# Optimization experiments

Measured on AMD Instinct MI355X. Metric: run time of the kernel, lower is better.

## Reference

```python
import jax, jax.numpy as jnp
import numpy as np

DIM = 768
H = 12        # query heads
HKV = 4       # kv heads
G = H // HKV  # GQA group size
HD = 64       # head dim
CAP = 50.0    # soft cap (Gemma-2 style)
EPS = 1e-6
SCALE = HD ** -0.5
B, T, S = 1, 128, 256


def setup_inputs() -> dict:
    key = jax.random.key(0)
    ks = jax.random.split(key, 5)
    s = DIM ** -0.5
    x = jax.random.normal(ks[0], (B, T, S, DIM), jnp.float32)
    Wq = jax.random.normal(ks[1], (DIM, H * HD), jnp.float32) * s
    Wk = jax.random.normal(ks[2], (DIM, HKV * HD), jnp.float32) * s
    Wv = jax.random.normal(ks[3], (DIM, HKV * HD), jnp.float32) * s
    Wo = jax.random.normal(ks[4], (H * HD, DIM), jnp.float32) * s
    q_norm_w = jnp.ones((HD,), jnp.float32)
    k_norm_w = jnp.ones((HD,), jnp.float32)
    return {"x": x, "Wq": Wq, "Wk": Wk, "Wv": Wv, "Wo": Wo,
            "q_norm_w": q_norm_w, "k_norm_w": k_norm_w}


def _rmsnorm(x, w):
    # x: (..., HD)
    return x * jax.lax.rsqrt(jnp.mean(x * x, axis=-1, keepdims=True) + EPS) * w


def reference(x, Wq, Wk, Wv, Wo, q_norm_w, k_norm_w):
    b, t, s, d = x.shape
    n = b * s
    # fold spatial into batch: temporal attention per spatial position
    xf = x.transpose(0, 2, 1, 3).reshape(n, t, d)             # (N, T, D)
    q = (xf @ Wq).reshape(n, t, H, HD).transpose(0, 2, 1, 3)   # (N, H, T, hd)
    k = (xf @ Wk).reshape(n, t, HKV, HD).transpose(0, 2, 1, 3) # (N, Hkv, T, hd)
    v = (xf @ Wv).reshape(n, t, HKV, HD).transpose(0, 2, 1, 3)
    # QKNorm (per-head RMSNorm on head_dim)
    q = _rmsnorm(q, q_norm_w)
    k = _rmsnorm(k, k_norm_w)
    # GQA without materializing repeated K/V: split q heads into (Hkv, G)
    # (repeat_interleave maps query head h -> kv head h // G, matching kv*G+g)
    qg = q.reshape(n, HKV, G, t, HD)
    attn = jnp.einsum('bkgtd,bksd->bkgts', qg, k) * SCALE      # (N, Hkv, G, T, T)
    attn = CAP * jnp.tanh(attn / CAP)                          # soft cap
    causal = jnp.triu(jnp.ones((t, t), bool), 1)               # True above diag
    attn = jnp.where(causal, -jnp.inf, attn)
    attn = jax.nn.softmax(attn, axis=-1)
    out = jnp.einsum('bkgts,bksd->bkgtd', attn, v)             # (N, Hkv, G, T, hd)
    out = out.reshape(n, H, t, HD).transpose(0, 2, 1, 3).reshape(n, t, H * HD)
    out = out @ Wo                                             # (N, T, D)
    return out.reshape(b, s, t, d).transpose(0, 2, 1, 3)        # (B, T, S, D)
```

## Files before the change

kernel.cpp:

```cpp
#include <hip/hip_runtime.h>
#include <stdint.h>
#include <stddef.h>

#define DIM 768
#define NH  12
#define NKV 4
#define HD  64
#define TT  128
#define NS  256

typedef __attribute__((ext_vector_type(8))) short bf16x8;
typedef __attribute__((ext_vector_type(4))) float f32x4;
typedef __attribute__((ext_vector_type(4))) unsigned int u32x4;
typedef __attribute__((ext_vector_type(2))) unsigned int u32x2;

__device__ __forceinline__ unsigned short f2bf(float f) {
  union { float f; unsigned int u; } v; v.f = f;
  return (unsigned short)((v.u + 0x7FFFu + ((v.u >> 16) & 1u)) >> 16);
}

__device__ __forceinline__ void gload_lds16(const void* g, void* l) {
  __builtin_amdgcn_global_load_lds(
      (const __attribute__((address_space(1))) unsigned int*)g,
      (__attribute__((address_space(3))) unsigned int*)l, 16, 0, 0);
}

__global__ __launch_bounds__(256)
void prep_kernel(const float* __restrict__ x, const float* __restrict__ Wq,
                 const float* __restrict__ Wk, const float* __restrict__ Wv,
                 const float* __restrict__ Wo, unsigned short* __restrict__ Wt,
                 unsigned short* __restrict__ WoT, unsigned short* __restrict__ xb) {
  const int b = blockIdx.x, tid = threadIdx.x;
  if (b < 6144) {
    int idx = b * 256 + tid;
    const int n1 = 1280 * DIM;
    if (idx < n1) {
      int c = idx / DIM, kk = idx - c * DIM;
      float v;
      if (c < 768)       v = Wq[kk * 768 + c];
      else if (c < 1024) v = Wk[kk * 256 + (c - 768)];
      else               v = Wv[kk * 256 + (c - 1024)];
      Wt[idx] = f2bf(v);
    } else {
      int i2 = idx - n1;
      int c = i2 / DIM, kk = i2 - c * DIM;
      WoT[i2] = f2bf(Wo[kk * 768 + c]);
    }
  } else {
    int g = (b - 6144) * 256 + tid;
    int r = g / 192;
    int k = g - r * 192;
    int t = r >> 8, n = r & 255;
    f32x4 f = *reinterpret_cast<const f32x4*>(x + (size_t)g * 4);
    u32x2 pk;
    pk[0] = (unsigned)f2bf(f[0]) | ((unsigned)f2bf(f[1]) << 16);
    pk[1] = (unsigned)f2bf(f[2]) | ((unsigned)f2bf(f[3]) << 16);
    *reinterpret_cast<u32x2*>(xb + (size_t)((n << 7) + t) * DIM + k * 4) = pk;
  }
}

__global__ __launch_bounds__(512, 2)
void qkv_kernel(const unsigned short* __restrict__ xb, const float* __restrict__ qnw,
                const float* __restrict__ knw, const unsigned short* __restrict__ Wt,
                unsigned short* __restrict__ qb, unsigned short* __restrict__ kb,
                unsigned short* __restrict__ vTb) {
  extern __shared__ unsigned short lds[];
  const int b = blockIdx.x;
  const int x8 = b & 7, idx = b >> 3;
  const int cbt = idx % 5;
  const int n   = (idx / 5) * 8 + x8;
  const int tid = threadIdx.x;
  const int wave = tid >> 6, lane = tid & 63;
  const int cl = lane & 15, rowg = lane >> 4;
  const int wmw = wave >> 2, wn = wave & 3;
  const int l8 = lane >> 3, s8 = lane & 7;
  const int col0 = cbt * 256;
  const unsigned short* asrc = xb + (size_t)(n * TT + l8) * DIM + (s8 ^ l8) * 8;
  const unsigned short* bsrc = Wt + (size_t)(col0 + l8) * DIM + (s8 ^ l8) * 8;
  const int swzr = (cl & 7) << 4;
  f32x4 acc[4][4] = {};

#define QKV_STAGE(buf, ko)                                                  \
  {                                                                         \
    unsigned short* Ad = lds + (buf) * 24576;                               \
    unsigned short* Bd = Ad + 8192;                                         \
    _Pragma("unroll")                                                       \
    for (int i = 0; i < 2; ++i) {                                           \
      const int r0 = i * 64 + wave * 8;                                     \
      gload_lds16(asrc + (size_t)r0 * DIM + (ko), Ad + r0 * 64);            \
    }                                                                       \
    _Pragma("unroll")                                                       \
    for (int i = 0; i < 4; ++i) {                                           \
      const int r0 = i * 64 + wave * 8;                                     \
      gload_lds16(bsrc + (size_t)r0 * DIM + (ko), Bd + r0 * 64);            \
    }                                                                       \
  }

  QKV_STAGE(0, 0);
  __syncthreads();
  for (int kt = 0; kt < 12; ++kt) {
    if (kt < 11) QKV_STAGE((kt + 1) & 1, (kt + 1) * 64);
    const char* Ab = (const char*)(lds + (kt & 1) * 24576);
    const char* Bb = Ab + 16384;
    #pragma unroll
    for (int ks = 0; ks < 2; ++ks) {
      bf16x8 a[4], bb[4];
      #pragma unroll
      for (int m = 0; m < 4; ++m)
        a[m] = *(const bf16x8*)(Ab + (wmw * 64 + m * 16 + cl) * 128 + ((ks * 64 + rowg * 16) ^ swzr));
      #pragma unroll
      for (int nn = 0; nn < 4; ++nn)
        bb[nn] = *(const bf16x8*)(Bb + (wn * 64 + nn * 16 + cl) * 128 + ((ks * 64 + rowg * 16) ^ swzr));
      #pragma unroll
      for (int m = 0; m < 4; ++m)
        #pragma unroll
        for (int nn = 0; nn < 4; ++nn)
          acc[m][nn] = __builtin_amdgcn_mfma_f32_16x16x32_bf16(a[m], bb[nn], acc[m][nn], 0, 0, 0);
    }
    __syncthreads();
  }

  if (cbt == 4) {
    const int kv = wn;
    unsigned short* dst = vTb + (size_t)((n * NKV + kv) * HD) * TT;
    #pragma unroll
    for (int m = 0; m < 4; ++m) {
      const int tb = wmw * 64 + m * 16 + rowg * 4;
      #pragma unroll
      for (int nn = 0; nn < 4; ++nn) {
        const int d = nn * 16 + cl;
        u32x2 pk;
        pk[0] = (unsigned)f2bf(acc[m][nn][0]) | ((unsigned)f2bf(acc[m][nn][1]) << 16);
        pk[1] = (unsigned)f2bf(acc[m][nn][2]) | ((unsigned)f2bf(acc[m][nn][3]) << 16);
        *reinterpret_cast<u32x2*>(dst + (size_t)d * TT + tb) = pk;
      }
    }
  } else {
    const int isq = (cbt < 3);
    const float* nw = isq ? qnw : knw;
    float wfrag[4];
    #pragma unroll
    for (int nn = 0; nn < 4; ++nn) wfrag[nn] = nw[nn * 16 + cl];
    const float rs = isq ? 0.125f : 1.0f;
    unsigned short* dst;
    if (isq) { const int hh = cbt * 4 + wn; dst = qb + (size_t)(n * NH + hh) * TT * HD; }
    else     { const int kv = wn;           dst = kb + (size_t)(n * NKV + kv) * TT * HD; }
    #pragma unroll
    for (int m = 0; m < 4; ++m) {
      #pragma unroll
      for (int j = 0; j < 4; ++j) {
        const int t = wmw * 64 + m * 16 + rowg * 4 + j;
        float ss = 0.f;
        #pragma unroll
        for (int nn = 0; nn < 4; ++nn) { float v = acc[m][nn][j]; ss += v * v; }
        #pragma unroll
        for (int dlt = 1; dlt < 16; dlt <<= 1) ss += __shfl_xor(ss, dlt);
        const float r = rsqrtf(ss * (1.f / 64.f) + 1e-6f) * rs;
        #pragma unroll
        for (int nn = 0; nn < 4; ++nn)
          dst[(size_t)t * HD + nn * 16 + cl] = f2bf(acc[m][nn][j] * r * wfrag[nn]);
      }
    }
  }
#undef QKV_STAGE
}

__global__ __launch_bounds__(256)
void attn_kernel(const unsigned short* __restrict__ qb, const unsigned short* __restrict__ kb,
                 const unsigned short* __restrict__ vTb, unsigned short* __restrict__ ab) {
  extern __shared__ char smem[];
  unsigned short (*Ks)[72]   = reinterpret_cast<unsigned short (*)[72]>(smem);
  unsigned short (*Vts)[136] = reinterpret_cast<unsigned short (*)[136]>(smem + 18432);
  unsigned short (*Pl)[136]  = reinterpret_cast<unsigned short (*)[136]>(smem + 35840);
  const int b = blockIdx.x;
  const int x8 = b & 7, idx = b >> 3;
  const int kv = idx & 3;
  const int n  = (idx >> 2) * 8 + x8;
  const int tid = threadIdx.x, wave = tid >> 6, lane = tid & 63;
  const int cl = lane & 15, rowg = lane >> 4;

  const unsigned short* ksrc = kb + (size_t)(n * NKV + kv) * TT * HD;
  const unsigned short* vsrc = vTb + (size_t)(n * NKV + kv) * HD * TT;
  #pragma unroll
  for (int i = 0; i < 4; ++i) {
    int c = tid + 256 * i, r = c >> 3, seg = c & 7;
    *reinterpret_cast<u32x4*>(&Ks[r][seg * 8]) = *reinterpret_cast<const u32x4*>(ksrc + c * 8);
  }
  #pragma unroll
  for (int i = 0; i < 4; ++i) {
    int c = tid + 256 * i, r = c >> 4, seg = c & 15;
    *reinterpret_cast<u32x4*>(&Vts[r][seg * 8]) = *reinterpret_cast<const u32x4*>(vsrc + c * 8);
  }
  __syncthreads();

  for (int hh = 0; hh < 3; ++hh) {
    const int h = kv * 3 + hh;
    const unsigned short* qsrc = qb + (size_t)(n * NH + h) * TT * HD;
    f32x4 sc[2][8] = {};
    #pragma unroll
    for (int ks = 0; ks < 2; ++ks) {
      bf16x8 a[2], bbf[8];
      #pragma unroll
      for (int m = 0; m < 2; ++m)
        a[m] = *reinterpret_cast<const bf16x8*>(
            qsrc + (size_t)(wave * 32 + m * 16 + cl) * HD + ks * 32 + rowg * 8);
      #pragma unroll
      for (int nn = 0; nn < 8; ++nn)
        bbf[nn] = *reinterpret_cast<const bf16x8*>(&Ks[nn * 16 + cl][ks * 32 + rowg * 8]);
      #pragma unroll
      for (int m = 0; m < 2; ++m)
        #pragma unroll
        for (int nn = 0; nn < 8; ++nn)
          sc[m][nn] = __builtin_amdgcn_mfma_f32_16x16x32_bf16(a[m], bbf[nn], sc[m][nn], 0, 0, 0);
    }
    #pragma unroll
    for (int m = 0; m < 2; ++m) {
      #pragma unroll
      for (int j = 0; j < 4; ++j) {
        const int rowv = wave * 32 + m * 16 + rowg * 4 + j;
        float mx = -__builtin_inff();
        #pragma unroll
        for (int nn = 0; nn < 8; ++nn) {
          float s = sc[m][nn][j];
          float e = __expf(s * 0.04f);
          s = 50.f - 100.f * __builtin_amdgcn_rcpf(e + 1.f);
          if (nn * 16 + cl > rowv) s = -__builtin_inff();
          sc[m][nn][j] = s;
          mx = fmaxf(mx, s);
        }
        #pragma unroll
        for (int d = 1; d < 16; d <<= 1) mx = fmaxf(mx, __shfl_xor(mx, d));
        float sum = 0.f;
        #pragma unroll
        for (int nn = 0; nn < 8; ++nn) {
          float e = __expf(sc[m][nn][j] - mx);
          sc[m][nn][j] = e;
          sum += e;
        }
        #pragma unroll
        for (int d = 1; d < 16; d <<= 1) sum += __shfl_xor(sum, d);
        const float inv = __builtin_amdgcn_rcpf(sum);
        #pragma unroll
        for (int nn = 0; nn < 8; ++nn)
          Pl[rowv][nn * 16 + cl] = f2bf(sc[m][nn][j] * inv);
      }
    }
    __syncthreads();
    f32x4 o[2][4] = {};
    #pragma unroll
    for (int ks = 0; ks < 4; ++ks) {
      bf16x8 a[2], bbf[4];
      #pragma unroll
      for (int m = 0; m < 2; ++m)
        a[m] = *reinterpret_cast<const bf16x8*>(&Pl[wave * 32 + m * 16 + cl][ks * 32 + rowg * 8]);
      #pragma unroll
      for (int nn = 0; nn < 4; ++nn)
        bbf[nn] = *reinterpret_cast<const bf16x8*>(&Vts[nn * 16 + cl][ks * 32 + rowg * 8]);
      #pragma unroll
      for (int m = 0; m < 2; ++m)
        #pragma unroll
        for (int nn = 0; nn < 4; ++nn)
          o[m][nn] = __builtin_amdgcn_mfma_f32_16x16x32_bf16(a[m], bbf[nn], o[m][nn], 0, 0, 0);
    }
    unsigned short* dst = ab + (size_t)n * TT * DIM + h * HD;
    #pragma unroll
    for (int m = 0; m < 2; ++m)
      #pragma unroll
      for (int j = 0; j < 4; ++j) {
        int t = wave * 32 + m * 16 + rowg * 4 + j;
        #pragma unroll
        for (int nn = 0; nn < 4; ++nn)
          dst[(size_t)t * DIM + nn * 16 + cl] = f2bf(o[m][nn][j]);
      }
    __syncthreads();
  }
}

__global__ __launch_bounds__(512, 2)
void out_kernel(const unsigned short* __restrict__ ab, const unsigned short* __restrict__ WoT,
                float* __restrict__ out) {
  extern __shared__ unsigned short lds[];
  const int b = blockIdx.x;
  const int x8 = b & 7, idx = b >> 3;
  const int cbt = idx % 3;
  const int n   = (idx / 3) * 8 + x8;
  const int tid = threadIdx.x;
  const int wave = tid >> 6, lane = tid & 63;
  const int cl = lane & 15, rowg = lane >> 4;
  const int wmw = wave >> 2, wn = wave & 3;
  const int l8 = lane >> 3, s8 = lane & 7;
  const unsigned short* asrc = ab  + (size_t)(n * TT + l8) * DIM + (s8 ^ l8) * 8;
  const unsigned short* bsrc = WoT + (size_t)(cbt * 256 + l8) * DIM + (s8 ^ l8) * 8;
  const int swzr = (cl & 7) << 4;
  f32x4 acc[4][4] = {};

#define OUT_STAGE(buf, ko)                                                  \
  {                                                                         \
    unsigned short* Ad = lds + (buf) * 24576;                               \
    unsigned short* Bd = Ad + 8192;                                         \
    _Pragma("unroll")                                                       \
    for (int i = 0; i < 2; ++i) {                                           \
      const int r0 = i * 64 + wave * 8;                                     \
      gload_lds16(asrc + (size_t)r0 * DIM + (ko), Ad + r0 * 64);            \
    }                                                                       \
    _Pragma("unroll")                                                       \
    for (int i = 0; i < 4; ++i) {                                           \
      const int r0 = i * 64 + wave * 8;                                     \
      gload_lds16(bsrc + (size_t)r0 * DIM + (ko), Bd + r0 * 64);            \
    }                                                                       \
  }

  OUT_STAGE(0, 0);
  __syncthreads();
  for (int kt = 0; kt < 12; ++kt) {
    if (kt < 11) OUT_STAGE((kt + 1) & 1, (kt + 1) * 64);
    const char* Ab = (const char*)(lds + (kt & 1) * 24576);
    const char* Bb = Ab + 16384;
    #pragma unroll
    for (int ks = 0; ks < 2; ++ks) {
      bf16x8 a[4], bb[4];
      #pragma unroll
      for (int m = 0; m < 4; ++m)
        a[m] = *(const bf16x8*)(Ab + (wmw * 64 + m * 16 + cl) * 128 + ((ks * 64 + rowg * 16) ^ swzr));
      #pragma unroll
      for (int nn = 0; nn < 4; ++nn)
        bb[nn] = *(const bf16x8*)(Bb + (wn * 64 + nn * 16 + cl) * 128 + ((ks * 64 + rowg * 16) ^ swzr));
      #pragma unroll
      for (int m = 0; m < 4; ++m)
        #pragma unroll
        for (int nn = 0; nn < 4; ++nn)
          acc[m][nn] = __builtin_amdgcn_mfma_f32_16x16x32_bf16(a[m], bb[nn], acc[m][nn], 0, 0, 0);
    }
    __syncthreads();
  }
  #pragma unroll
  for (int m = 0; m < 4; ++m)
    #pragma unroll
    for (int j = 0; j < 4; ++j) {
      int t = wmw * 64 + m * 16 + rowg * 4 + j;
      #pragma unroll
      for (int nn = 0; nn < 4; ++nn)
        out[(size_t)(t * NS + n) * DIM + cbt * 256 + wn * 64 + nn * 16 + cl] = acc[m][nn][j];
    }
#undef OUT_STAGE
}

extern "C" void kernel_launch(void* const* d_in, const int* in_sizes, int n_in,
                              void* d_out, int out_size, void* d_ws, size_t ws_size,
                              hipStream_t stream) {
  const float* x   = (const float*)d_in[0];
  const float* Wq  = (const float*)d_in[1];
  const float* Wk  = (const float*)d_in[2];
  const float* Wv  = (const float*)d_in[3];
  const float* Wo  = (const float*)d_in[4];
  const float* qnw = (const float*)d_in[5];
  const float* knw = (const float*)d_in[6];
  (void)in_sizes; (void)n_in; (void)out_size;

  char* ws = (char*)d_ws;
  unsigned short* Wt  = (unsigned short*)(ws + 0);
  unsigned short* WoT = (unsigned short*)(ws + 1966080);
  unsigned short* qb  = (unsigned short*)(ws + 3145728);
  unsigned short* kb  = (unsigned short*)(ws + 53477376);
  unsigned short* vTb = (unsigned short*)(ws + 70254592);
  unsigned short* ab  = (unsigned short*)(ws + 87031808);
  unsigned short* xb  = ab;
  if (ws_size < 137363456) return;

  hipFuncSetAttribute(reinterpret_cast<const void*>(qkv_kernel),
                      hipFuncAttributeMaxDynamicSharedMemorySize, 98304);
  hipFuncSetAttribute(reinterpret_cast<const void*>(out_kernel),
                      hipFuncAttributeMaxDynamicSharedMemorySize, 98304);
  hipFuncSetAttribute(reinterpret_cast<const void*>(attn_kernel),
                      hipFuncAttributeMaxDynamicSharedMemorySize, 70656);

  prep_kernel<<<30720, 256, 0, stream>>>(x, Wq, Wk, Wv, Wo, Wt, WoT, xb);
  qkv_kernel<<<1280, 512, 98304, stream>>>(xb, qnw, knw, Wt, qb, kb, vTb);
  attn_kernel<<<1024, 256, 70656, stream>>>(qb, kb, vTb, ab);
  out_kernel<<<768, 512, 98304, stream>>>(ab, WoT, (float*)d_out);
}
```

Before: 219.5 us.

## Triple-buffer GEMM K-loop with one barrier; stage Q/K epilogue through LDS

Both projection GEMMs (QKV and output) move from a double-buffered K-loop with two __syncthreads per step to a three-stage LDS ring. Each step waits with an explicit s_waitcnt vmcnt and uses one s_barrier, so global-to-LDS loads run two tiles ahead and one barrier per iteration is removed. The Q/K normalized epilogue now writes its bf16 results into LDS and then copies them out with 16-byte coalesced stores, replacing scattered 2-byte global stores. Dynamic LDS rises from 96KB to 144KB per block, which rules out running two blocks per CU and depends on hand-written vmcnt counts matching the per-stage load count.

```diff
diff --git a/kernel.cpp b/kernel.cpp
--- a/kernel.cpp
+++ b/kernel.cpp
@@ -74,9 +74,8 @@
   const int cl = lane & 15, rowg = lane >> 4;
   const int wmw = wave >> 2, wn = wave & 3;
   const int l8 = lane >> 3, s8 = lane & 7;
-  const int col0 = cbt * 256;
   const unsigned short* asrc = xb + (size_t)(n * TT + l8) * DIM + (s8 ^ l8) * 8;
-  const unsigned short* bsrc = Wt + (size_t)(col0 + l8) * DIM + (s8 ^ l8) * 8;
+  const unsigned short* bsrc = Wt + (size_t)(cbt * 256 + l8) * DIM + (s8 ^ l8) * 8;
   const int swzr = (cl & 7) << 4;
   f32x4 acc[4][4] = {};
 
@@ -97,10 +96,15 @@
   }
 
   QKV_STAGE(0, 0);
-  __syncthreads();
+  QKV_STAGE(1, 64);
+  #pragma unroll
   for (int kt = 0; kt < 12; ++kt) {
-    if (kt < 11) QKV_STAGE((kt + 1) & 1, (kt + 1) * 64);
-    const char* Ab = (const char*)(lds + (kt & 1) * 24576);
+    if (kt < 11) asm volatile("s_waitcnt vmcnt(6)" ::: "memory");
+    else         asm volatile("s_waitcnt vmcnt(0)" ::: "memory");
+    __builtin_amdgcn_s_barrier();
+    __builtin_amdgcn_sched_barrier(0);
+    if (kt + 2 < 12) QKV_STAGE((kt + 2) % 3, (kt + 2) * 64);
+    const char* Ab = (const char*)(lds + (kt % 3) * 24576);
     const char* Bb = Ab + 16384;
     #pragma unroll
     for (int ks = 0; ks < 2; ++ks) {
@@ -117,8 +121,9 @@
         for (int nn = 0; nn < 4; ++nn)
           acc[m][nn] = __builtin_amdgcn_mfma_f32_16x16x32_bf16(a[m], bb[nn], acc[m][nn], 0, 0, 0);
     }
-    __syncthreads();
-  }
+  }
+#undef QKV_STAGE
+  __syncthreads();
 
   if (cbt == 4) {
     const int kv = wn;
@@ -142,9 +147,6 @@
     #pragma unroll
     for (int nn = 0; nn < 4; ++nn) wfrag[nn] = nw[nn * 16 + cl];
     const float rs = isq ? 0.125f : 1.0f;
-    unsigned short* dst;
-    if (isq) { const int hh = cbt * 4 + wn; dst = qb + (size_t)(n * NH + hh) * TT * HD; }
-    else     { const int kv = wn;           dst = kb + (size_t)(n * NKV + kv) * TT * HD; }
     #pragma unroll
     for (int m = 0; m < 4; ++m) {
       #pragma unroll
@@ -158,11 +160,18 @@
         const float r = rsqrtf(ss * (1.f / 64.f) + 1e-6f) * rs;
         #pragma unroll
         for (int nn = 0; nn < 4; ++nn)
-          dst[(size_t)t * HD + nn * 16 + cl] = f2bf(acc[m][nn][j] * r * wfrag[nn]);
+          lds[wn * 8192 + t * 64 + nn * 16 + cl] = f2bf(acc[m][nn][j] * r * wfrag[nn]);
       }
     }
-  }
-#undef QKV_STAGE
+    __syncthreads();
+    unsigned short* gdst = isq ? qb + ((size_t)n * NH + cbt * 4) * TT * HD
+                               : kb + (size_t)n * NKV * TT * HD;
+    #pragma unroll
+    for (int i = 0; i < 8; ++i) {
+      const int c = tid + 512 * i;
+      *reinterpret_cast<u32x4*>(gdst + c * 8) = *reinterpret_cast<const u32x4*>(lds + c * 8);
+    }
+  }
 }
 
 __global__ __launch_bounds__(256)
@@ -311,10 +320,15 @@
   }
 
   OUT_STAGE(0, 0);
-  __syncthreads();
+  OUT_STAGE(1, 64);
+  #pragma unroll
   for (int kt = 0; kt < 12; ++kt) {
-    if (kt < 11) OUT_STAGE((kt + 1) & 1, (kt + 1) * 64);
-    const char* Ab = (const char*)(lds + (kt & 1) * 24576);
+    if (kt < 11) asm volatile("s_waitcnt vmcnt(6)" ::: "memory");
+    else         asm volatile("s_waitcnt vmcnt(0)" ::: "memory");
+    __builtin_amdgcn_s_barrier();
+    __builtin_amdgcn_sched_barrier(0);
+    if (kt + 2 < 12) OUT_STAGE((kt + 2) % 3, (kt + 2) * 64);
+    const char* Ab = (const char*)(lds + (kt % 3) * 24576);
     const char* Bb = Ab + 16384;
     #pragma unroll
     for (int ks = 0; ks < 2; ++ks) {
@@ -331,8 +345,8 @@
         for (int nn = 0; nn < 4; ++nn)
           acc[m][nn] = __builtin_amdgcn_mfma_f32_16x16x32_bf16(a[m], bb[nn], acc[m][nn], 0, 0, 0);
     }
-    __syncthreads();
-  }
+  }
+#undef OUT_STAGE
   #pragma unroll
   for (int m = 0; m < 4; ++m)
     #pragma unroll
@@ -342,7 +356,6 @@
       for (int nn = 0; nn < 4; ++nn)
         out[(size_t)(t * NS + n) * DIM + cbt * 256 + wn * 64 + nn * 16 + cl] = acc[m][nn][j];
     }
-#undef OUT_STAGE
 }
 
 extern "C" void kernel_launch(void* const* d_in, const int* in_sizes, int n_in,
@@ -368,14 +381,14 @@
   if (ws_size < 137363456) return;
 
   hipFuncSetAttribute(reinterpret_cast<const void*>(qkv_kernel),
-                      hipFuncAttributeMaxDynamicSharedMemorySize, 98304);
+                      hipFuncAttributeMaxDynamicSharedMemorySize, 147456);
   hipFuncSetAttribute(reinterpret_cast<const void*>(out_kernel),
-                      hipFuncAttributeMaxDynamicSharedMemorySize, 98304);
+                      hipFuncAttributeMaxDynamicSharedMemorySize, 147456);
   hipFuncSetAttribute(reinterpret_cast<const void*>(attn_kernel),
                       hipFuncAttributeMaxDynamicSharedMemorySize, 70656);
 
   prep_kernel<<<30720, 256, 0, stream>>>(x, Wq, Wk, Wv, Wo, Wt, WoT, xb);
-  qkv_kernel<<<1280, 512, 98304, stream>>>(xb, qnw, knw, Wt, qb, kb, vTb);
+  qkv_kernel<<<1280, 512, 147456, stream>>>(xb, qnw, knw, Wt, qb, kb, vTb);
   attn_kernel<<<1024, 256, 70656, stream>>>(qb, kb, vTb, ab);
-  out_kernel<<<768, 512, 98304, stream>>>(ab, WoT, (float*)d_out);
-}
+  out_kernel<<<768, 512, 147456, stream>>>(ab, WoT, (float*)d_out);
+}
```

Result: no change. 223.2 us (+1.7%).

## Fuse x fp32-to-bf16 conversion into QKV GEMM loads and stage Q/K stores via LDS

Applied to the files above, without the earlier changes.

The separate pass in the prep kernel that converted and transposed x to bf16 is removed. The QKV GEMM now reads fp32 x directly with register prefetch, converts it, and writes swizzled bf16 tiles to LDS, while B tiles still use async global-to-LDS loads. This saves a full write and read of the bf16 copy of x. The cost is that each of the five column-tile blocks per position re-reads fp32 x, doubling A-operand bytes per tile. Q/K results are also staged in LDS and written out with coalesced 16-byte stores instead of scattered 2-byte stores.

```diff
diff --git a/kernel.cpp b/kernel.cpp
--- a/kernel.cpp
+++ b/kernel.cpp
@@ -26,41 +26,27 @@
 }
 
 __global__ __launch_bounds__(256)
-void prep_kernel(const float* __restrict__ x, const float* __restrict__ Wq,
-                 const float* __restrict__ Wk, const float* __restrict__ Wv,
-                 const float* __restrict__ Wo, unsigned short* __restrict__ Wt,
-                 unsigned short* __restrict__ WoT, unsigned short* __restrict__ xb) {
-  const int b = blockIdx.x, tid = threadIdx.x;
-  if (b < 6144) {
-    int idx = b * 256 + tid;
-    const int n1 = 1280 * DIM;
-    if (idx < n1) {
-      int c = idx / DIM, kk = idx - c * DIM;
-      float v;
-      if (c < 768)       v = Wq[kk * 768 + c];
-      else if (c < 1024) v = Wk[kk * 256 + (c - 768)];
-      else               v = Wv[kk * 256 + (c - 1024)];
-      Wt[idx] = f2bf(v);
-    } else {
-      int i2 = idx - n1;
-      int c = i2 / DIM, kk = i2 - c * DIM;
-      WoT[i2] = f2bf(Wo[kk * 768 + c]);
-    }
+void prep_kernel(const float* __restrict__ Wq, const float* __restrict__ Wk,
+                 const float* __restrict__ Wv, const float* __restrict__ Wo,
+                 unsigned short* __restrict__ Wt, unsigned short* __restrict__ WoT) {
+  int idx = blockIdx.x * 256 + threadIdx.x;
+  const int n1 = 1280 * DIM;
+  if (idx < n1) {
+    int c = idx / DIM, kk = idx - c * DIM;
+    float v;
+    if (c < 768)       v = Wq[kk * 768 + c];
+    else if (c < 1024) v = Wk[kk * 256 + (c - 768)];
+    else               v = Wv[kk * 256 + (c - 1024)];
+    Wt[idx] = f2bf(v);
   } else {
-    int g = (b - 6144) * 256 + tid;
-    int r = g / 192;
-    int k = g - r * 192;
-    int t = r >> 8, n = r & 255;
-    f32x4 f = *reinterpret_cast<const f32x4*>(x + (size_t)g * 4);
-    u32x2 pk;
-    pk[0] = (unsigned)f2bf(f[0]) | ((unsigned)f2bf(f[1]) << 16);
-    pk[1] = (unsigned)f2bf(f[2]) | ((unsigned)f2bf(f[3]) << 16);
-    *reinterpret_cast<u32x2*>(xb + (size_t)((n << 7) + t) * DIM + k * 4) = pk;
+    int i2 = idx - n1;
+    int c = i2 / DIM, kk = i2 - c * DIM;
+    WoT[i2] = f2bf(Wo[kk * 768 + c]);
   }
 }
 
 __global__ __launch_bounds__(512, 2)
-void qkv_kernel(const unsigned short* __restrict__ xb, const float* __restrict__ qnw,
+void qkv_kernel(const float* __restrict__ x, const float* __restrict__ qnw,
                 const float* __restrict__ knw, const unsigned short* __restrict__ Wt,
                 unsigned short* __restrict__ qb, unsigned short* __restrict__ kb,
                 unsigned short* __restrict__ vTb) {
@@ -74,32 +60,48 @@
   const int cl = lane & 15, rowg = lane >> 4;
   const int wmw = wave >> 2, wn = wave & 3;
   const int l8 = lane >> 3, s8 = lane & 7;
-  const int col0 = cbt * 256;
-  const unsigned short* asrc = xb + (size_t)(n * TT + l8) * DIM + (s8 ^ l8) * 8;
-  const unsigned short* bsrc = Wt + (size_t)(col0 + l8) * DIM + (s8 ^ l8) * 8;
+  const unsigned short* bsrc = Wt + (size_t)(cbt * 256 + l8) * DIM + (s8 ^ l8) * 8;
   const int swzr = (cl & 7) << 4;
+  const int r0 = tid >> 3, s0 = tid & 7;
+  const float* ax0 = x + (size_t)(r0 * NS + n) * DIM + s0 * 8;
+  const float* ax1 = x + (size_t)((r0 + 64) * NS + n) * DIM + s0 * 8;
+  const int wd0 = r0 * 128 + ((s0 * 16) ^ ((r0 & 7) << 4));
+  const int wd1 = (r0 + 64) * 128 + ((s0 * 16) ^ ((r0 & 7) << 4));
   f32x4 acc[4][4] = {};
-
-#define QKV_STAGE(buf, ko)                                                  \
-  {                                                                         \
-    unsigned short* Ad = lds + (buf) * 24576;                               \
-    unsigned short* Bd = Ad + 8192;                                         \
-    _Pragma("unroll")                                                       \
-    for (int i = 0; i < 2; ++i) {                                           \
-      const int r0 = i * 64 + wave * 8;                                     \
-      gload_lds16(asrc + (size_t)r0 * DIM + (ko), Ad + r0 * 64);            \
-    }                                                                       \
-    _Pragma("unroll")                                                       \
-    for (int i = 0; i < 4; ++i) {                                           \
-      const int r0 = i * 64 + wave * 8;                                     \
-      gload_lds16(bsrc + (size_t)r0 * DIM + (ko), Bd + r0 * 64);            \
-    }                                                                       \
-  }
-
-  QKV_STAGE(0, 0);
+  f32x4 aL0, aL1, aL2, aL3;
+
+#define QKV_STAGE_B(bufp, ko) {                                              \
+    unsigned short* Bd = lds + (bufp) * 24576 + 8192;                        \
+    gload_lds16(bsrc + (size_t)(wave * 8) * DIM + (ko), Bd + (wave * 8) * 64);            \
+    gload_lds16(bsrc + (size_t)(64 + wave * 8) * DIM + (ko), Bd + (64 + wave * 8) * 64);  \
+    gload_lds16(bsrc + (size_t)(128 + wave * 8) * DIM + (ko), Bd + (128 + wave * 8) * 64);\
+    gload_lds16(bsrc + (size_t)(192 + wave * 8) * DIM + (ko), Bd + (192 + wave * 8) * 64); }
+#define QKV_A_LOAD(ko) {                                                     \
+    aL0 = *reinterpret_cast<const f32x4*>(ax0 + (ko));                       \
+    aL1 = *reinterpret_cast<const f32x4*>(ax0 + (ko) + 4);                   \
+    aL2 = *reinterpret_cast<const f32x4*>(ax1 + (ko));                       \
+    aL3 = *reinterpret_cast<const f32x4*>(ax1 + (ko) + 4); }
+#define QKV_A_WRITE(bufp) {                                                  \
+    unsigned short* Ad = lds + (bufp) * 24576;                               \
+    u32x4 p0, p1;                                                            \
+    p0[0] = (unsigned)f2bf(aL0[0]) | ((unsigned)f2bf(aL0[1]) << 16);         \
+    p0[1] = (unsigned)f2bf(aL0[2]) | ((unsigned)f2bf(aL0[3]) << 16);         \
+    p0[2] = (unsigned)f2bf(aL1[0]) | ((unsigned)f2bf(aL1[1]) << 16);         \
+    p0[3] = (unsigned)f2bf(aL1[2]) | ((unsigned)f2bf(aL1[3]) << 16);         \
+    p1[0] = (unsigned)f2bf(aL2[0]) | ((unsigned)f2bf(aL2[1]) << 16);         \
+    p1[1] = (unsigned)f2bf(aL2[2]) | ((unsigned)f2bf(aL2[3]) << 16);         \
+    p1[2] = (unsigned)f2bf(aL3[0]) | ((unsigned)f2bf(aL3[1]) << 16);         \
+    p1[3] = (unsigned)f2bf(aL3[2]) | ((unsigned)f2bf(aL3[3]) << 16);         \
+    *reinterpret_cast<u32x4*>((char*)Ad + wd0) = p0;                         \
+    *reinterpret_cast<u32x4*>((char*)Ad + wd1) = p1; }
+
+  QKV_A_LOAD(0);
+  QKV_STAGE_B(0, 0);
+  QKV_A_WRITE(0);
   __syncthreads();
   for (int kt = 0; kt < 12; ++kt) {
-    if (kt < 11) QKV_STAGE((kt + 1) & 1, (kt + 1) * 64);
+    const int nxt = (kt + 1) & 1;
+    if (kt < 11) { QKV_A_LOAD((kt + 1) * 64); QKV_STAGE_B(nxt, (kt + 1) * 64); }
     const char* Ab = (const char*)(lds + (kt & 1) * 24576);
     const char* Bb = Ab + 16384;
     #pragma unroll
@@ -117,8 +119,13 @@
         for (int nn = 0; nn < 4; ++nn)
           acc[m][nn] = __builtin_amdgcn_mfma_f32_16x16x32_bf16(a[m], bb[nn], acc[m][nn], 0, 0, 0);
     }
-    __syncthreads();
-  }
+    if (kt < 11) QKV_A_WRITE(nxt);
+    __syncthreads();
+  }
+#undef QKV_STAGE_B
+#undef QKV_A_LOAD
+#undef QKV_A_WRITE
+  __syncthreads();
 
   if (cbt == 4) {
     const int kv = wn;
@@ -142,9 +149,7 @@
     #pragma unroll
     for (int nn = 0; nn < 4; ++nn) wfrag[nn] = nw[nn * 16 + cl];
     const float rs = isq ? 0.125f : 1.0f;
-    unsigned short* dst;
-    if (isq) { const int hh = cbt * 4 + wn; dst = qb + (size_t)(n * NH + hh) * TT * HD; }
-    else     { const int kv = wn;           dst = kb + (size_t)(n * NKV + kv) * TT * HD; }
+    unsigned short* slab = lds + wn * 8192;
     #pragma unroll
     for (int m = 0; m < 4; ++m) {
       #pragma unroll
@@ -158,11 +163,18 @@
         const float r = rsqrtf(ss * (1.f / 64.f) + 1e-6f) * rs;
         #pragma unroll
         for (int nn = 0; nn < 4; ++nn)
-          dst[(size_t)t * HD + nn * 16 + cl] = f2bf(acc[m][nn][j] * r * wfrag[nn]);
+          slab[t * 64 + nn * 16 + cl] = f2bf(acc[m][nn][j] * r * wfrag[nn]);
       }
     }
-  }
-#undef QKV_STAGE
+    __syncthreads();
+    unsigned short* gdst = isq ? qb + ((size_t)n * NH + cbt * 4) * TT * HD
+                               : kb + (size_t)n * NKV * TT * HD;
+    #pragma unroll
+    for (int i = 0; i < 8; ++i) {
+      const int c = tid + 512 * i;
+      *reinterpret_cast<u32x4*>(gdst + c * 8) = *reinterpret_cast<const u32x4*>(lds + c * 8);
+    }
+  }
 }
 
 __global__ __launch_bounds__(256)
@@ -300,13 +312,13 @@
     unsigned short* Bd = Ad + 8192;                                         \
     _Pragma("unroll")                                                       \
     for (int i = 0; i < 2; ++i) {                                           \
-      const int r0 = i * 64 + wave * 8;                                     \
-      gload_lds16(asrc + (size_t)r0 * DIM + (ko), Ad + r0 * 64);            \
+      const int rr = i * 64 + wave * 8;                                     \
+      gload_lds16(asrc + (size_t)rr * DIM + (ko), Ad + rr * 64);            \
     }                                                                       \
     _Pragma("unroll")                                                       \
     for (int i = 0; i < 4; ++i) {                                           \
-      const int r0 = i * 64 + wave * 8;                                     \
-      gload_lds16(bsrc + (size_t)r0 * DIM + (ko), Bd + r0 * 64);            \
+      const int rr = i * 64 + wave * 8;                                     \
+      gload_lds16(bsrc + (size_t)rr * DIM + (ko), Bd + rr * 64);            \
     }                                                                       \
   }
 
@@ -333,6 +345,7 @@
     }
     __syncthreads();
   }
+#undef OUT_STAGE
   #pragma unroll
   for (int m = 0; m < 4; ++m)
     #pragma unroll
@@ -342,7 +355,6 @@
       for (int nn = 0; nn < 4; ++nn)
         out[(size_t)(t * NS + n) * DIM + cbt * 256 + wn * 64 + nn * 16 + cl] = acc[m][nn][j];
     }
-#undef OUT_STAGE
 }
 
 extern "C" void kernel_launch(void* const* d_in, const int* in_sizes, int n_in,
@@ -364,7 +376,6 @@
   unsigned short* kb  = (unsigned short*)(ws + 53477376);
   unsigned short* vTb = (unsigned short*)(ws + 70254592);
   unsigned short* ab  = (unsigned short*)(ws + 87031808);
-  unsigned short* xb  = ab;
   if (ws_size < 137363456) return;
 
   hipFuncSetAttribute(reinterpret_cast<const void*>(qkv_kernel),
@@ -374,8 +385,8 @@
   hipFuncSetAttribute(reinterpret_cast<const void*>(attn_kernel),
                       hipFuncAttributeMaxDynamicSharedMemorySize, 70656);
 
-  prep_kernel<<<30720, 256, 0, stream>>>(x, Wq, Wk, Wv, Wo, Wt, WoT, xb);
-  qkv_kernel<<<1280, 512, 98304, stream>>>(xb, qnw, knw, Wt, qb, kb, vTb);
+  prep_kernel<<<6144, 256, 0, stream>>>(Wq, Wk, Wv, Wo, Wt, WoT);
+  qkv_kernel<<<1280, 512, 98304, stream>>>(x, qnw, knw, Wt, qb, kb, vTb);
   attn_kernel<<<1024, 256, 70656, stream>>>(qb, kb, vTb, ab);
   out_kernel<<<768, 512, 98304, stream>>>(ab, WoT, (float*)d_out);
 }
```

Measured after the change: 246.1 us. +12.1%, slower.

## Parallelize attention heads across waves instead of a serial per-head loop

Applied to the files above, without the earlier changes.

The attention kernel now runs 6 waves per block, one per (query head of the GQA group, 64-row half), instead of 4 waves looping over the three heads. Each wave gets a private P buffer in LDS, which removes the per-head __syncthreads barriers and the serial head loop. The cost is a much larger LDS footprint (about 140 KB per block), which likely limits the kernel to one block per CU. It also raises per-wave register use, with larger score and output accumulators.

```diff
diff --git a/kernel.cpp b/kernel.cpp
--- a/kernel.cpp
+++ b/kernel.cpp
@@ -74,9 +74,8 @@
   const int cl = lane & 15, rowg = lane >> 4;
   const int wmw = wave >> 2, wn = wave & 3;
   const int l8 = lane >> 3, s8 = lane & 7;
-  const int col0 = cbt * 256;
   const unsigned short* asrc = xb + (size_t)(n * TT + l8) * DIM + (s8 ^ l8) * 8;
-  const unsigned short* bsrc = Wt + (size_t)(col0 + l8) * DIM + (s8 ^ l8) * 8;
+  const unsigned short* bsrc = Wt + (size_t)(cbt * 256 + l8) * DIM + (s8 ^ l8) * 8;
   const int swzr = (cl & 7) << 4;
   f32x4 acc[4][4] = {};
 
@@ -86,13 +85,13 @@
     unsigned short* Bd = Ad + 8192;                                         \
     _Pragma("unroll")                                                       \
     for (int i = 0; i < 2; ++i) {                                           \
-      const int r0 = i * 64 + wave * 8;                                     \
-      gload_lds16(asrc + (size_t)r0 * DIM + (ko), Ad + r0 * 64);            \
+      const int rr = i * 64 + wave * 8;                                     \
+      gload_lds16(asrc + (size_t)rr * DIM + (ko), Ad + rr * 64);            \
     }                                                                       \
     _Pragma("unroll")                                                       \
     for (int i = 0; i < 4; ++i) {                                           \
-      const int r0 = i * 64 + wave * 8;                                     \
-      gload_lds16(bsrc + (size_t)r0 * DIM + (ko), Bd + r0 * 64);            \
+      const int rr = i * 64 + wave * 8;                                     \
+      gload_lds16(bsrc + (size_t)rr * DIM + (ko), Bd + rr * 64);            \
     }                                                                       \
   }
 
@@ -119,6 +118,7 @@
     }
     __syncthreads();
   }
+#undef QKV_STAGE
 
   if (cbt == 4) {
     const int kv = wn;
@@ -162,118 +162,118 @@
       }
     }
   }
-#undef QKV_STAGE
-}
-
-__global__ __launch_bounds__(256)
+}
+
+__global__ __launch_bounds__(384)
 void attn_kernel(const unsigned short* __restrict__ qb, const unsigned short* __restrict__ kb,
                  const unsigned short* __restrict__ vTb, unsigned short* __restrict__ ab) {
   extern __shared__ char smem[];
   unsigned short (*Ks)[72]   = reinterpret_cast<unsigned short (*)[72]>(smem);
   unsigned short (*Vts)[136] = reinterpret_cast<unsigned short (*)[136]>(smem + 18432);
-  unsigned short (*Pl)[136]  = reinterpret_cast<unsigned short (*)[136]>(smem + 35840);
   const int b = blockIdx.x;
   const int x8 = b & 7, idx = b >> 3;
   const int kv = idx & 3;
   const int n  = (idx >> 2) * 8 + x8;
   const int tid = threadIdx.x, wave = tid >> 6, lane = tid & 63;
   const int cl = lane & 15, rowg = lane >> 4;
+  const int h     = kv * 3 + (wave >> 1);
+  const int rbase = (wave & 1) * 64;
 
   const unsigned short* ksrc = kb + (size_t)(n * NKV + kv) * TT * HD;
   const unsigned short* vsrc = vTb + (size_t)(n * NKV + kv) * HD * TT;
-  #pragma unroll
-  for (int i = 0; i < 4; ++i) {
-    int c = tid + 256 * i, r = c >> 3, seg = c & 7;
-    *reinterpret_cast<u32x4*>(&Ks[r][seg * 8]) = *reinterpret_cast<const u32x4*>(ksrc + c * 8);
-  }
-  #pragma unroll
-  for (int i = 0; i < 4; ++i) {
-    int c = tid + 256 * i, r = c >> 4, seg = c & 15;
-    *reinterpret_cast<u32x4*>(&Vts[r][seg * 8]) = *reinterpret_cast<const u32x4*>(vsrc + c * 8);
+  if (tid < 256) {
+    #pragma unroll
+    for (int i = 0; i < 4; ++i) {
+      int c = tid + 256 * i, r = c >> 3, seg = c & 7;
+      *reinterpret_cast<u32x4*>(&Ks[r][seg * 8]) = *reinterpret_cast<const u32x4*>(ksrc + c * 8);
+    }
+    #pragma unroll
+    for (int i = 0; i < 4; ++i) {
+      int c = tid + 256 * i, r = c >> 4, seg = c & 15;
+      *reinterpret_cast<u32x4*>(&Vts[r][seg * 8]) = *reinterpret_cast<const u32x4*>(vsrc + c * 8);
+    }
   }
   __syncthreads();
 
-  for (int hh = 0; hh < 3; ++hh) {
-    const int h = kv * 3 + hh;
-    const unsigned short* qsrc = qb + (size_t)(n * NH + h) * TT * HD;
-    f32x4 sc[2][8] = {};
-    #pragma unroll
-    for (int ks = 0; ks < 2; ++ks) {
-      bf16x8 a[2], bbf[8];
-      #pragma unroll
-      for (int m = 0; m < 2; ++m)
-        a[m] = *reinterpret_cast<const bf16x8*>(
-            qsrc + (size_t)(wave * 32 + m * 16 + cl) * HD + ks * 32 + rowg * 8);
+  const unsigned short* qsrc = qb + (size_t)(n * NH + h) * TT * HD;
+  f32x4 sc[4][8] = {};
+  #pragma unroll
+  for (int ks = 0; ks < 2; ++ks) {
+    bf16x8 a[4], bbf[8];
+    #pragma unroll
+    for (int m = 0; m < 4; ++m)
+      a[m] = *reinterpret_cast<const bf16x8*>(
+          qsrc + (size_t)(rbase + m * 16 + cl) * HD + ks * 32 + rowg * 8);
+    #pragma unroll
+    for (int nn = 0; nn < 8; ++nn)
+      bbf[nn] = *reinterpret_cast<const bf16x8*>(&Ks[nn * 16 + cl][ks * 32 + rowg * 8]);
+    #pragma unroll
+    for (int m = 0; m < 4; ++m)
       #pragma unroll
       for (int nn = 0; nn < 8; ++nn)
-        bbf[nn] = *reinterpret_cast<const bf16x8*>(&Ks[nn * 16 + cl][ks * 32 + rowg * 8]);
-      #pragma unroll
-      for (int m = 0; m < 2; ++m)
-        #pragma unroll
-        for (int nn = 0; nn < 8; ++nn)
-          sc[m][nn] = __builtin_amdgcn_mfma_f32_16x16x32_bf16(a[m], bbf[nn], sc[m][nn], 0, 0, 0);
-    }
-    #pragma unroll
-    for (int m = 0; m < 2; ++m) {
-      #pragma unroll
-      for (int j = 0; j < 4; ++j) {
-        const int rowv = wave * 32 + m * 16 + rowg * 4 + j;
-        float mx = -__builtin_inff();
-        #pragma unroll
-        for (int nn = 0; nn < 8; ++nn) {
-          float s = sc[m][nn][j];
-          float e = __expf(s * 0.04f);
-          s = 50.f - 100.f * __builtin_amdgcn_rcpf(e + 1.f);
-          if (nn * 16 + cl > rowv) s = -__builtin_inff();
-          sc[m][nn][j] = s;
-          mx = fmaxf(mx, s);
-        }
-        #pragma unroll
-        for (int d = 1; d < 16; d <<= 1) mx = fmaxf(mx, __shfl_xor(mx, d));
-        float sum = 0.f;
-        #pragma unroll
-        for (int nn = 0; nn < 8; ++nn) {
-          float e = __expf(sc[m][nn][j] - mx);
-          sc[m][nn][j] = e;
-          sum += e;
-        }
-        #pragma unroll
-        for (int d = 1; d < 16; d <<= 1) sum += __shfl_xor(sum, d);
-        const float inv = __builtin_amdgcn_rcpf(sum);
-        #pragma unroll
-        for (int nn = 0; nn < 8; ++nn)
-          Pl[rowv][nn * 16 + cl] = f2bf(sc[m][nn][j] * inv);
+        sc[m][nn] = __builtin_amdgcn_mfma_f32_16x16x32_bf16(a[m], bbf[nn], sc[m][nn], 0, 0, 0);
+  }
+  unsigned short (*Pl)[136] =
+      reinterpret_cast<unsigned short (*)[136]>(smem + 35840 + wave * 17408);
+  #pragma unroll
+  for (int m = 0; m < 4; ++m) {
+    #pragma unroll
+    for (int j = 0; j < 4; ++j) {
+      const int rloc = m * 16 + rowg * 4 + j;
+      const int rowv = rbase + rloc;
+      float mx = -__builtin_inff();
+      #pragma unroll
+      for (int nn = 0; nn < 8; ++nn) {
+        float s = sc[m][nn][j];
+        float e = __expf(s * 0.04f);
+        s = 50.f - 100.f * __builtin_amdgcn_rcpf(e + 1.f);
+        if (nn * 16 + cl > rowv) s = -__builtin_inff();
+        sc[m][nn][j] = s;
+        mx = fmaxf(mx, s);
       }
-    }
-    __syncthreads();
-    f32x4 o[2][4] = {};
-    #pragma unroll
-    for (int ks = 0; ks < 4; ++ks) {
-      bf16x8 a[2], bbf[4];
-      #pragma unroll
-      for (int m = 0; m < 2; ++m)
-        a[m] = *reinterpret_cast<const bf16x8*>(&Pl[wave * 32 + m * 16 + cl][ks * 32 + rowg * 8]);
-      #pragma unroll
-      for (int nn = 0; nn < 4; ++nn)
-        bbf[nn] = *reinterpret_cast<const bf16x8*>(&Vts[nn * 16 + cl][ks * 32 + rowg * 8]);
-      #pragma unroll
-      for (int m = 0; m < 2; ++m)
-        #pragma unroll
-        for (int nn = 0; nn < 4; ++nn)
-          o[m][nn] = __builtin_amdgcn_mfma_f32_16x16x32_bf16(a[m], bbf[nn], o[m][nn], 0, 0, 0);
-    }
-    unsigned short* dst = ab + (size_t)n * TT * DIM + h * HD;
-    #pragma unroll
-    for (int m = 0; m < 2; ++m)
-      #pragma unroll
-      for (int j = 0; j < 4; ++j) {
-        int t = wave * 32 + m * 16 + rowg * 4 + j;
-        #pragma unroll
-        for (int nn = 0; nn < 4; ++nn)
-          dst[(size_t)t * DIM + nn * 16 + cl] = f2bf(o[m][nn][j]);
+      #pragma unroll
+      for (int d = 1; d < 16; d <<= 1) mx = fmaxf(mx, __shfl_xor(mx, d));
+      float sum = 0.f;
+      #pragma unroll
+      for (int nn = 0; nn < 8; ++nn) {
+        float e = __expf(sc[m][nn][j] - mx);
+        sc[m][nn][j] = e;
+        sum += e;
       }
-    __syncthreads();
-  }
+      #pragma unroll
+      for (int d = 1; d < 16; d <<= 1) sum += __shfl_xor(sum, d);
+      const float inv = __builtin_amdgcn_rcpf(sum);
+      #pragma unroll
+      for (int nn = 0; nn < 8; ++nn)
+        Pl[rloc][nn * 16 + cl] = f2bf(sc[m][nn][j] * inv);
+    }
+  }
+  f32x4 o[4][4] = {};
+  #pragma unroll
+  for (int ks = 0; ks < 4; ++ks) {
+    bf16x8 a[4], bbf[4];
+    #pragma unroll
+    for (int m = 0; m < 4; ++m)
+      a[m] = *reinterpret_cast<const bf16x8*>(&Pl[m * 16 + cl][ks * 32 + rowg * 8]);
+    #pragma unroll
+    for (int nn = 0; nn < 4; ++nn)
+      bbf[nn] = *reinterpret_cast<const bf16x8*>(&Vts[nn * 16 + cl][ks * 32 + rowg * 8]);
+    #pragma unroll
+    for (int m = 0; m < 4; ++m)
+      #pragma unroll
+      for (int nn = 0; nn < 4; ++nn)
+        o[m][nn] = __builtin_amdgcn_mfma_f32_16x16x32_bf16(a[m], bbf[nn], o[m][nn], 0, 0, 0);
+  }
+  unsigned short* dst = ab + (size_t)n * TT * DIM + h * HD;
+  #pragma unroll
+  for (int m = 0; m < 4; ++m)
+    #pragma unroll
+    for (int j = 0; j < 4; ++j) {
+      const int t = rbase + m * 16 + rowg * 4 + j;
+      #pragma unroll
+      for (int nn = 0; nn < 4; ++nn)
+        dst[(size_t)t * DIM + nn * 16 + cl] = f2bf(o[m][nn][j]);
+    }
 }
 
 __global__ __launch_bounds__(512, 2)
@@ -300,13 +300,13 @@
     unsigned short* Bd = Ad + 8192;                                         \
     _Pragma("unroll")                                                       \
     for (int i = 0; i < 2; ++i) {                                           \
-      const int r0 = i * 64 + wave * 8;                                     \
-      gload_lds16(asrc + (size_t)r0 * DIM + (ko), Ad + r0 * 64);            \
+      const int rr = i * 64 + wave * 8;                                     \
+      gload_lds16(asrc + (size_t)rr * DIM + (ko), Ad + rr * 64);            \
     }                                                                       \
     _Pragma("unroll")                                                       \
     for (int i = 0; i < 4; ++i) {                                           \
-      const int r0 = i * 64 + wave * 8;                                     \
-      gload_lds16(bsrc + (size_t)r0 * DIM + (ko), Bd + r0 * 64);            \
+      const int rr = i * 64 + wave * 8;                                     \
+      gload_lds16(bsrc + (size_t)rr * DIM + (ko), Bd + rr * 64);            \
     }                                                                       \
   }
 
@@ -333,6 +333,7 @@
     }
     __syncthreads();
   }
+#undef OUT_STAGE
   #pragma unroll
   for (int m = 0; m < 4; ++m)
     #pragma unroll
@@ -342,7 +343,6 @@
       for (int nn = 0; nn < 4; ++nn)
         out[(size_t)(t * NS + n) * DIM + cbt * 256 + wn * 64 + nn * 16 + cl] = acc[m][nn][j];
     }
-#undef OUT_STAGE
 }
 
 extern "C" void kernel_launch(void* const* d_in, const int* in_sizes, int n_in,
@@ -372,10 +372,10 @@
   hipFuncSetAttribute(reinterpret_cast<const void*>(out_kernel),
                       hipFuncAttributeMaxDynamicSharedMemorySize, 98304);
   hipFuncSetAttribute(reinterpret_cast<const void*>(attn_kernel),
-                      hipFuncAttributeMaxDynamicSharedMemorySize, 70656);
+                      hipFuncAttributeMaxDynamicSharedMemorySize, 140288);
 
   prep_kernel<<<30720, 256, 0, stream>>>(x, Wq, Wk, Wv, Wo, Wt, WoT, xb);
   qkv_kernel<<<1280, 512, 98304, stream>>>(xb, qnw, knw, Wt, qb, kb, vTb);
-  attn_kernel<<<1024, 256, 70656, stream>>>(qb, kb, vTb, ab);
+  attn_kernel<<<1024, 384, 140288, stream>>>(qb, kb, vTb, ab);
   out_kernel<<<768, 512, 98304, stream>>>(ab, WoT, (float*)d_out);
 }
```

New measurement: 226.8 us. 1.03x slower.
